# Optimization experiments

Hardware: AMD Instinct MI355X
Metric: run time of the kernel (lower is better)

## Reference

```python
import jax, jax.numpy as jnp
import numpy as np

D, H, DH, FF = 768, 12, 64, 3072

def setup_inputs() -> dict:
    key = jax.random.key(0)
    ks = iter(jax.random.split(key, 40))
    B, Li, Lt = 128, 197, 64
    nrm = lambda shape, s=0.02: (jax.random.normal(next(ks), shape, jnp.float32) * s)
    inp = {}
    inp['image_feats'] = jax.random.normal(next(ks), (B, Li, D), jnp.float32)
    inp['image_att_score'] = jax.random.uniform(next(ks), (B, Li), jnp.float32)
    inp['text_feats'] = jax.random.normal(next(ks), (B, Lt, D), jnp.float32)
    inp['text_att_score'] = jax.random.uniform(next(ks), (B, Lt), jnp.float32)
    inp['tokens'] = jax.random.randint(next(ks), (B, Lt), 0, 1000)
    # BatchNorm1d bottlenecks (inference: running stats)
    for p in ('img', 'txt'):
        inp[f'bn_{p}_g'] = jnp.ones((D,), jnp.float32)
        inp[f'bn_{p}_b'] = jnp.zeros((D,), jnp.float32)
        inp[f'bn_{p}_m'] = nrm((D,), 0.1)
        inp[f'bn_{p}_v'] = jax.random.uniform(next(ks), (D,), jnp.float32, 0.5, 1.5)
    # ResidualAttention (1 layer, cross): ln1, ln2, qkv/out proj, mlp 768->3072->768
    inp['ln1_g'] = jnp.ones((D,), jnp.float32); inp['ln1_b'] = jnp.zeros((D,), jnp.float32)
    inp['ln2_g'] = jnp.ones((D,), jnp.float32); inp['ln2_b'] = jnp.zeros((D,), jnp.float32)
    for n in ('Wq', 'Wk', 'Wv', 'Wo'):
        inp[n] = nrm((D, D))
    for n in ('bq', 'bk', 'bv', 'bo'):
        inp[n] = jnp.zeros((D,), jnp.float32)
    inp['W1'] = nrm((D, FF)); inp['b1'] = jnp.zeros((FF,), jnp.float32)
    inp['W2'] = nrm((FF, D)); inp['b2'] = jnp.zeros((D,), jnp.float32)
    inp['img_K'] = 59   # int(197 * 0.3)
    inp['text_K'] = 19  # int(64 * 0.3)
    return inp

def _ln(x, g, b):
    mu = jnp.mean(x, -1, keepdims=True)
    v = jnp.mean((x - mu) ** 2, -1, keepdims=True)
    return (x - mu) * jax.lax.rsqrt(v + 1e-5) * g + b

def _bn(x, g, b, m, v):
    return (x - m) * jax.lax.rsqrt(v + 1e-5) * g + b

def _cross_block(x, y, key_mask, ln1_g, ln1_b, ln2_g, ln2_b,
                 Wq, bq, Wk, bk, Wv, bv, Wo, bo, W1, b1, W2, b2):
    # cross-attn: queries from x, keys/values from y; pre-LN residual block
    B, Lq, _ = x.shape
    Lk = y.shape[1]
    qn = _ln(x, ln1_g, ln1_b)
    kn = _ln(y, ln1_g, ln1_b)
    q = (qn @ Wq + bq).reshape(B, Lq, H, DH)
    k = (kn @ Wk + bk).reshape(B, Lk, H, DH)
    v = (kn @ Wv + bv).reshape(B, Lk, H, DH)
    scores = jnp.einsum('bqhd,bkhd->bhqk', q, k) / np.float32(np.sqrt(DH))
    if key_mask is not None:  # True = padding -> masked out
        scores = jnp.where(key_mask[:, None, None, :], jnp.float32(-1e9), scores)
    a = jax.nn.softmax(scores, axis=-1)
    att = jnp.einsum('bhqk,bkhd->bqhd', a, v).reshape(B, Lq, D) @ Wo + bo
    x = x + att
    h = _ln(x, ln2_g, ln2_b)
    x = x + jax.nn.gelu(h @ W1 + b1, approximate=False) @ W2 + b2
    return x

def _select(feats, score, K):
    # zero CLS score, full descending sort via top_k, gather token subsets
    L = score.shape[1]
    score = score * jnp.concatenate([jnp.zeros_like(score[:, :1]), jnp.ones_like(score[:, 1:])], axis=1)
    _, idx = jax.lax.top_k(score, L)  # [B, L] sorted desc
    cls = feats[:, :1, :]
    sel1 = jnp.take_along_axis(feats, idx[:, :K, None], axis=1)
    sel2 = jnp.take_along_axis(feats, idx[:, K:2 * K, None], axis=1)
    return jnp.concatenate([cls, sel1], 1), jnp.concatenate([cls, sel2], 1)

def reference(image_feats, image_att_score, text_feats, text_att_score, tokens,
              bn_img_g, bn_img_b, bn_img_m, bn_img_v,
              bn_txt_g, bn_txt_b, bn_txt_m, bn_txt_v,
              ln1_g, ln1_b, ln2_g, ln2_b,
              Wq, bq, Wk, bk, Wv, bv, Wo, bo, W1, b1, W2, b2,
              img_K, text_K):
    blk = lambda x, y, m: _cross_block(x, y, m, ln1_g, ln1_b, ln2_g, ln2_b,
                                       Wq, bq, Wk, bk, Wv, bv, Wo, bo, W1, b1, W2, b2)
    img_global = _bn(image_feats[:, 0, :], bn_img_g, bn_img_b, bn_img_m, bn_img_v)
    text_global = _bn(text_feats[:, 0, :], bn_txt_g, bn_txt_b, bn_txt_m, bn_txt_v)
    text_masks = (tokens == 0)  # True where padding
    img_sel1, img_sel2 = _select(image_feats, image_att_score, img_K)
    image_part1 = blk(img_sel1, image_feats, None)
    image_part2 = blk(img_sel2, image_feats, None)
    txt_sel1, txt_sel2 = _select(text_feats, text_att_score, text_K)
    text_part1 = blk(txt_sel1, text_feats, text_masks)
    text_part2 = blk(txt_sel2, text_feats, text_masks)
    return (img_global, text_global, image_part1, image_part2, text_part1, text_part2)
```

## Files before the change

kernel.cpp:

```cpp
#include <hip/hip_runtime.h>

typedef unsigned short u16;
typedef __bf16 bf16x8 __attribute__((ext_vector_type(8)));
typedef float f32x4 __attribute__((ext_vector_type(4)));

__device__ __forceinline__ float b2f(u16 u) { return __builtin_bit_cast(float, (unsigned)u << 16); }
__device__ __forceinline__ u16 f2b(float f) {
  unsigned x = __builtin_bit_cast(unsigned, f);
  x += 0x7fffu + ((x >> 16) & 1u);
  return (u16)(x >> 16);
}

__device__ __forceinline__ void gload16(const u16* g, u16* l) {
  auto gp = (__attribute__((address_space(1))) void*)(void*)const_cast<u16*>(g);
  auto lp = (__attribute__((address_space(3))) void*)(void*)l;
  __builtin_amdgcn_global_load_lds(gp, lp, 16, 0, 0);
}

__device__ __forceinline__ f32x4 mfma16(bf16x8 a, bf16x8 b, f32x4 c) {
  return __builtin_amdgcn_mfma_f32_16x16x32_bf16(a, b, c, 0, 0, 0);
}

__device__ __forceinline__ float gelu_fast(float v) {
  float u = v * (0.7978845608028654f + 0.03567740813636141f * v * v);
  float e = __expf(2.0f * u);
  float th = 1.0f - 2.0f / (e + 1.0f);
  return 0.5f * v * (1.0f + th);
}

__global__ __launch_bounds__(256) void transpose_k(const float* __restrict__ in, u16* __restrict__ out,
                                                   int R, int C) {
  __shared__ float tile[32][33];
  const int bx = blockIdx.x * 32, by = blockIdx.y * 32;
  const int x = threadIdx.x;
  for (int yy = threadIdx.y; yy < 32; yy += 8) tile[yy][x] = in[(size_t)(by + yy) * C + bx + x];
  __syncthreads();
  for (int yy = threadIdx.y; yy < 32; yy += 8) out[(size_t)(bx + yy) * R + by + x] = f2b(tile[x][yy]);
}

__global__ __launch_bounds__(256) void transpose4(const float* __restrict__ i0, const float* __restrict__ i1,
                                                  const float* __restrict__ i2, const float* __restrict__ i3,
                                                  u16* __restrict__ o0, u16* __restrict__ o1,
                                                  u16* __restrict__ o2, u16* __restrict__ o3) {
  __shared__ float tile[32][33];
  const int z = blockIdx.z;
  const float* in = (z == 0) ? i0 : (z == 1) ? i1 : (z == 2) ? i2 : i3;
  u16* out = (z == 0) ? o0 : (z == 1) ? o1 : (z == 2) ? o2 : o3;
  const int bx = blockIdx.x * 32, by = blockIdx.y * 32;
  const int x = threadIdx.x;
  for (int yy = threadIdx.y; yy < 32; yy += 8) tile[yy][x] = in[(size_t)(by + yy) * 768 + bx + x];
  __syncthreads();
  for (int yy = threadIdx.y; yy < 32; yy += 8) out[(size_t)(bx + yy) * 768 + by + x] = f2b(tile[x][yy]);
}

__global__ __launch_bounds__(256) void bn_kernel(const float* __restrict__ feats, int Lrow,
                                                 const float* g, const float* b, const float* m, const float* v,
                                                 float* __restrict__ out) {
  const int bb = blockIdx.x;
  const float* row = feats + (size_t)bb * Lrow * 768;
  for (int d = threadIdx.x; d < 768; d += 256) {
    float x = row[d];
    out[bb * 768 + d] = (x - m[d]) * (1.0f / sqrtf(v[d] + 1e-5f)) * g[d] + b[d];
  }
}

__global__ __launch_bounds__(256) void topk_sel(const float* __restrict__ score, int L, int Ksel,
                                                int* __restrict__ sel, int Lq) {
  __shared__ float s[256];
  const int b = blockIdx.x;
  const int stride2 = 128 * Lq;
  for (int i = threadIdx.x; i < L; i += 256) {
    float v = score[b * L + i];
    s[i] = (i == 0) ? 0.0f : v;
  }
  __syncthreads();
  for (int i = threadIdx.x; i < L; i += 256) {
    float si = s[i];
    int rank = 0;
    for (int j = 0; j < L; ++j) {
      float sj = s[j];
      rank += (sj > si) || (sj == si && j < i);
    }
    if (rank < Ksel) sel[b * Lq + rank + 1] = i;
    else if (rank < 2 * Ksel) sel[stride2 + b * Lq + (rank - Ksel) + 1] = i;
  }
  if (threadIdx.x == 0) { sel[b * Lq] = 0; sel[stride2 + b * Lq] = 0; }
}

__global__ __launch_bounds__(256) void ln_rows(const float* __restrict__ x, const float* g, const float* b,
                                               u16* __restrict__ out) {
  const int row = blockIdx.x * 4 + (threadIdx.x >> 6);
  const int l = threadIdx.x & 63;
  const float* xr = x + (size_t)row * 768;
  float v[12]; float s = 0.f;
#pragma unroll
  for (int i = 0; i < 12; ++i) { v[i] = xr[l + i * 64]; s += v[i]; }
  for (int d = 1; d < 64; d <<= 1) s += __shfl_xor(s, d);
  const float mu = s * (1.0f / 768.0f);
  float q = 0.f;
#pragma unroll
  for (int i = 0; i < 12; ++i) { float t = v[i] - mu; q += t * t; }
  for (int d = 1; d < 64; d <<= 1) q += __shfl_xor(q, d);
  const float rs = 1.0f / sqrtf(q * (1.0f / 768.0f) + 1e-5f);
#pragma unroll
  for (int i = 0; i < 12; ++i) {
    int c = l + i * 64;
    out[(size_t)row * 768 + c] = f2b((v[i] - mu) * rs * g[c] + b[c]);
  }
}

__global__ __launch_bounds__(128) void gather_kernel(const int* __restrict__ sel, const u16* __restrict__ kn,
                                                     const float* __restrict__ feats, u16* __restrict__ qn,
                                                     float* __restrict__ xs, int Lq, int Lsrc) {
  const int q = blockIdx.x, by = blockIdx.y;
  const int p = by >> 7, b = by & 127;
  const int row = (p * 128 + b) * Lq + q;
  const int src = sel[row];
  const uint4* sq = (const uint4*)(kn + ((size_t)b * Lsrc + src) * 768);
  uint4* dq = (uint4*)(qn + (size_t)row * 768);
  for (int c = threadIdx.x; c < 96; c += 128) dq[c] = sq[c];
  const float4* sx = (const float4*)(feats + ((size_t)b * Lsrc + src) * 768);
  float4* dx = (float4*)(xs + (size_t)row * 768);
  for (int c = threadIdx.x; c < 192; c += 128) dx[c] = sx[c];
}

enum { EPI_PLAIN = 0, EPI_QSCALE = 1, EPI_GELU = 2, EPI_RES_FADD = 3, EPI_RES_OUT = 4 };

template <int EPI>
__device__ __forceinline__ void epi_write(float v, size_t off, void* outp, const float* res) {
  if constexpr (EPI == EPI_QSCALE) {
    ((u16*)outp)[off] = f2b(v * 0.125f);
  } else if constexpr (EPI == EPI_GELU) {
    ((u16*)outp)[off] = f2b(gelu_fast(v));
  } else if constexpr (EPI == EPI_RES_FADD || EPI == EPI_RES_OUT) {
    ((float*)outp)[off] = v + res[off];
  } else {
    ((u16*)outp)[off] = f2b(v);
  }
}

template <int EPI>
__global__ __launch_bounds__(256, 3) void gemm_bt(const u16* __restrict__ A, const u16* __restrict__ Bt,
                                                  const float* __restrict__ bias, const float* __restrict__ res,
                                                  void* __restrict__ outp, int M, int N, int K) {
  __shared__ alignas(16) u16 As[2][4096];
  __shared__ alignas(16) u16 Bs[2][4096];
  const int tid = threadIdx.x, l = tid & 63, w = tid >> 6;
  const int nwg = gridDim.x * gridDim.y;
  int lin = blockIdx.y * gridDim.x + blockIdx.x;
  const int q8 = nwg >> 3, r8 = nwg & 7;
  const int xcd = lin & 7, pos = lin >> 3;
  const int nl = (xcd < r8) ? (xcd * (q8 + 1) + pos) : (r8 * (q8 + 1) + (xcd - r8) * q8 + pos);
  const int m0 = (nl / gridDim.x) * 128, n0 = (nl % gridDim.x) * 128;
  const int wm = (w & 1) * 64, wn = (w >> 1) * 64;
  f32x4 acc[4][4] = {};

  int arow_g[2], ach_g[2];
#pragma unroll
  for (int p = 0; p < 2; ++p) {
    const int s = p * 256 + tid;
    const int rl = s >> 3, v = (s & 7) ^ (rl & 7);
    arow_g[p] = (v >> 2) * 64 + rl;
    ach_g[p] = (v & 3) * 8;
  }
  auto STAGE = [&](int buf, int k0) {
#pragma unroll
    for (int p = 0; p < 2; ++p) {
      const int s = p * 256 + tid;
      gload16(A + (size_t)(m0 + arow_g[p]) * K + k0 + ach_g[p], &As[buf][s * 8]);
      gload16(Bt + (size_t)(n0 + arow_g[p]) * K + k0 + ach_g[p], &Bs[buf][s * 8]);
    }
  };

  const int c = l >> 4;
  auto COMPUTE = [&](int buf) {
    bf16x8 af[4], bfr[4];
#pragma unroll
    for (int i = 0; i < 4; ++i) {
      const int arow = wm + i * 16 + (l & 15);
      const int slot = (c | ((arow >> 6) << 2)) ^ (arow & 7);
      af[i] = *(const bf16x8*)&As[buf][(arow & 63) * 64 + slot * 8];
      const int brow = wn + i * 16 + (l & 15);
      const int slotb = (c | ((brow >> 6) << 2)) ^ (brow & 7);
      bfr[i] = *(const bf16x8*)&Bs[buf][(brow & 63) * 64 + slotb * 8];
    }
    __builtin_amdgcn_s_setprio(1);
#pragma unroll
    for (int mi = 0; mi < 4; ++mi)
#pragma unroll
      for (int ni = 0; ni < 4; ++ni) acc[mi][ni] = mfma16(af[mi], bfr[ni], acc[mi][ni]);
    __builtin_amdgcn_s_setprio(0);
  };

  const int NT = K >> 5;
  STAGE(0, 0);
  int cur = 0;
  for (int t = 0; t < NT - 1; ++t) {
    STAGE(cur ^ 1, (t + 1) << 5);
    asm volatile("s_waitcnt vmcnt(4)" ::: "memory");
    __builtin_amdgcn_sched_barrier(0);
    __builtin_amdgcn_s_barrier();
    COMPUTE(cur);
    __builtin_amdgcn_s_barrier();
    cur ^= 1;
  }
  asm volatile("s_waitcnt vmcnt(0)" ::: "memory");
  __builtin_amdgcn_sched_barrier(0);
  __builtin_amdgcn_s_barrier();
  COMPUTE(cur);

  const int r4 = (l >> 4) * 4, c16 = l & 15;
#pragma unroll
  for (int mi = 0; mi < 4; ++mi)
#pragma unroll
    for (int ni = 0; ni < 4; ++ni) {
      const int gn = n0 + wn + ni * 16 + c16;
      const float bia = bias[gn];
#pragma unroll
      for (int j = 0; j < 4; ++j) {
        const int gm = m0 + wm + mi * 16 + r4 + j;
        epi_write<EPI>(acc[mi][ni][j] + bia, (size_t)gm * N + gn, outp, res);
      }
    }
}

template <int LQP, int LKP, int LQ, int LK, bool MASK>
__global__ __launch_bounds__(256) void attn2(const u16* __restrict__ Q, const u16* __restrict__ KVb,
                                             const int* __restrict__ toks, u16* __restrict__ O) {
  constexpr int LKS = LKP + 8;
  const int h = blockIdx.x, by = blockIdx.y;
  const int p = by & 1, bb = by >> 1;
  const int tid = threadIdx.x, l = tid & 63, w = tid >> 6;
  const size_t qrow0 = (size_t)(p * 128 + bb) * LQ;
  const u16* Qg = Q + qrow0 * 768 + h * 64;
  const u16* Kg = KVb + (size_t)bb * LK * 1536 + h * 64;
  const u16* Vg = Kg + 768;

  __shared__ alignas(16) u16 Qs[LQP * 64];
  __shared__ alignas(16) u16 KV[64 * LKS];
  __shared__ alignas(16) u16 Ss[LQP * LKS];
  __shared__ int tokLds[MASK ? LKP : 1];

  for (int s = tid; s < LQP * 8; s += 256) {
    int row = s >> 3, d8 = (s & 7) ^ (row & 7);
    int gr = row < LQ ? row : LQ - 1;
    gload16(Qg + (size_t)gr * 768 + d8 * 8, &Qs[s * 8]);
  }
  for (int s = tid; s < LKP * 8; s += 256) {
    int row = s >> 3, d8 = (s & 7) ^ (row & 7);
    int gr = row < LK ? row : LK - 1;
    gload16(Kg + (size_t)gr * 1536 + d8 * 8, &KV[s * 8]);
  }
  if (MASK)
    for (int c = tid; c < LKP; c += 256) tokLds[c] = (c < LK) ? toks[bb * LK + c] : 1;
  __syncthreads();

  for (int nt = w; nt < LKP / 16; nt += 4) {
    const int brow = nt * 16 + (l & 15);
#pragma unroll
    for (int mt = 0; mt < LQP / 16; ++mt) {
      const int arow = mt * 16 + (l & 15);
      f32x4 a_ = {0.f, 0.f, 0.f, 0.f};
#pragma unroll
      for (int kk = 0; kk < 2; ++kk) {
        bf16x8 av = *(const bf16x8*)&Qs[arow * 64 + (((kk * 4 + (l >> 4)) ^ (arow & 7)) << 3)];
        bf16x8 bv = *(const bf16x8*)&KV[brow * 64 + (((kk * 4 + (l >> 4)) ^ (brow & 7)) << 3)];
        a_ = mfma16(av, bv, a_);
      }
      const int r0 = mt * 16 + (l >> 4) * 4, cc = nt * 16 + (l & 15);
#pragma unroll
      for (int j = 0; j < 4; ++j) Ss[(r0 + j) * LKS + cc] = f2b(a_[j]);
    }
  }
  __syncthreads();

  {
    const int kcol = tid & 31, d8 = tid >> 5;
#pragma unroll
    for (int kb = 0; kb < LKP / 32; ++kb) {
      const int k = kb * 32 + kcol;
      alignas(16) u16 tmp[8] = {0, 0, 0, 0, 0, 0, 0, 0};
      if (k < LK) *(uint4*)tmp = *(const uint4*)(Vg + (size_t)k * 1536 + d8 * 8);
#pragma unroll
      for (int j = 0; j < 8; ++j) KV[(d8 * 8 + j) * LKS + k] = tmp[j];
    }
  }
  constexpr int NCH = (LKP + 63) / 64;
  for (int r = w; r < LQ; r += 4) {
    float sv[NCH];
    float mx = -INFINITY;
#pragma unroll
    for (int i = 0; i < NCH; ++i) {
      int c = l + (i << 6);
      float s = -INFINITY;
      if (c < LK) {
        s = b2f(Ss[r * LKS + c]);
        if (MASK && tokLds[c] == 0) s = -1e9f;
      }
      sv[i] = s;
      mx = fmaxf(mx, s);
    }
    for (int d = 1; d < 64; d <<= 1) mx = fmaxf(mx, __shfl_xor(mx, d));
    float sum = 0.f;
#pragma unroll
    for (int i = 0; i < NCH; ++i) { float e = __expf(sv[i] - mx); sv[i] = e; sum += e; }
    for (int d = 1; d < 64; d <<= 1) sum += __shfl_xor(sum, d);
    const float inv = 1.0f / sum;
#pragma unroll
    for (int i = 0; i < NCH; ++i) {
      int c = l + (i << 6);
      if (c < LKP) Ss[r * LKS + c] = f2b(sv[i] * inv);
    }
  }
  __syncthreads();

  for (int mt = w; mt < LQP / 16; mt += 4) {
    const int arow = mt * 16 + (l & 15);
#pragma unroll
    for (int nt = 0; nt < 4; ++nt) {
      f32x4 a_ = {0.f, 0.f, 0.f, 0.f};
#pragma unroll
      for (int kk = 0; kk < LKP; kk += 32) {
        bf16x8 av = *(const bf16x8*)&Ss[arow * LKS + kk + (l >> 4) * 8];
        bf16x8 bv = *(const bf16x8*)&KV[(nt * 16 + (l & 15)) * LKS + kk + (l >> 4) * 8];
        a_ = mfma16(av, bv, a_);
      }
      const int r0 = mt * 16 + (l >> 4) * 4, c16 = l & 15;
#pragma unroll
      for (int j = 0; j < 4; ++j) {
        int r = r0 + j;
        if (r < LQ) O[(qrow0 + r) * 768 + h * 64 + nt * 16 + c16] = f2b(a_[j]);
      }
    }
  }
}

extern "C" void kernel_launch(void* const* d_in, const int* in_sizes, int n_in,
                              void* d_out, int out_size, void* d_ws, size_t ws_size,
                              hipStream_t stream) {
  (void)in_sizes; (void)n_in; (void)out_size; (void)ws_size;
  const float* image_feats = (const float*)d_in[0];
  const float* image_att = (const float*)d_in[1];
  const float* text_feats = (const float*)d_in[2];
  const float* text_att = (const float*)d_in[3];
  const int* tokens = (const int*)d_in[4];
  const float* bn_img_g = (const float*)d_in[5];
  const float* bn_img_b = (const float*)d_in[6];
  const float* bn_img_m = (const float*)d_in[7];
  const float* bn_img_v = (const float*)d_in[8];
  const float* bn_txt_g = (const float*)d_in[9];
  const float* bn_txt_b = (const float*)d_in[10];
  const float* bn_txt_m = (const float*)d_in[11];
  const float* bn_txt_v = (const float*)d_in[12];
  const float* ln1_g = (const float*)d_in[13];
  const float* ln1_b = (const float*)d_in[14];
  const float* ln2_g = (const float*)d_in[15];
  const float* ln2_b = (const float*)d_in[16];
  const float* Wq = (const float*)d_in[17];
  const float* Wk = (const float*)d_in[18];
  const float* Wv = (const float*)d_in[19];
  const float* Wo = (const float*)d_in[20];
  const float* bq = (const float*)d_in[21];
  const float* bk = (const float*)d_in[22];
  const float* bv = (const float*)d_in[23];
  const float* bo = (const float*)d_in[24];
  const float* W1 = (const float*)d_in[25];
  const float* b1 = (const float*)d_in[26];
  const float* W2 = (const float*)d_in[27];
  const float* b2 = (const float*)d_in[28];

  float* out = (float*)d_out;
  char* wsp = (char*)d_ws;
  size_t off = 0;
  auto alloc = [&](size_t bytes) -> void* {
    void* p = wsp + off;
    off += (bytes + 255) & ~(size_t)255;
    return p;
  };
  u16* WqT = (u16*)alloc(768 * 768 * 2);
  u16* WkvT = (u16*)alloc((size_t)1536 * 768 * 2);
  u16* WoT = (u16*)alloc(768 * 768 * 2);
  u16* W1T = (u16*)alloc((size_t)768 * 3072 * 2);
  u16* W2T = (u16*)alloc((size_t)768 * 3072 * 2);
  float* bkv = (float*)alloc(1536 * 4);
  char* kvbase = (char*)(wsp + off);
  u16* kn_i = (u16*)alloc((size_t)25216 * 768 * 2);
  u16* KVb_i = (u16*)alloc((size_t)25216 * 1536 * 2);
  u16* kn_t = (u16*)alloc((size_t)8192 * 768 * 2);
  u16* KVb_t = (u16*)alloc((size_t)8192 * 1536 * 2);
  u16* gb = (u16*)kvbase;
  int* sel_i = (int*)alloc(2 * 128 * 60 * 4);
  int* sel_t = (int*)alloc(2 * 128 * 20 * 4);
  u16* qn = (u16*)alloc((size_t)20480 * 768 * 2);
  float* xs = (float*)alloc((size_t)20480 * 768 * 4);
  u16* Qb = (u16*)alloc((size_t)20480 * 768 * 2);

  const dim3 tb(32, 8);
  transpose4<<<dim3(24, 24, 4), tb, 0, stream>>>(Wq, Wk, Wv, Wo, WqT, WkvT, WkvT + (size_t)768 * 768, WoT);
  transpose_k<<<dim3(96, 24), tb, 0, stream>>>(W1, W1T, 768, 3072);
  transpose_k<<<dim3(24, 96), tb, 0, stream>>>(W2, W2T, 3072, 768);
  hipMemcpyAsync(bkv, bk, 768 * 4, hipMemcpyDeviceToDevice, stream);
  hipMemcpyAsync(bkv + 768, bv, 768 * 4, hipMemcpyDeviceToDevice, stream);

  bn_kernel<<<128, 256, 0, stream>>>(image_feats, 197, bn_img_g, bn_img_b, bn_img_m, bn_img_v, out);
  bn_kernel<<<128, 256, 0, stream>>>(text_feats, 64, bn_txt_g, bn_txt_b, bn_txt_m, bn_txt_v, out + 98304);

  topk_sel<<<128, 256, 0, stream>>>(image_att, 197, 59, sel_i, 60);
  topk_sel<<<128, 256, 0, stream>>>(text_att, 64, 19, sel_t, 20);

  ln_rows<<<25216 / 4, 256, 0, stream>>>(image_feats, ln1_g, ln1_b, kn_i);
  gemm_bt<EPI_PLAIN><<<dim3(12, 197), 256, 0, stream>>>(kn_i, WkvT, bkv, nullptr, KVb_i, 25216, 1536, 768);
  ln_rows<<<8192 / 4, 256, 0, stream>>>(text_feats, ln1_g, ln1_b, kn_t);
  gemm_bt<EPI_PLAIN><<<dim3(12, 64), 256, 0, stream>>>(kn_t, WkvT, bkv, nullptr, KVb_t, 8192, 1536, 768);

  gather_kernel<<<dim3(60, 256), 128, 0, stream>>>(sel_i, kn_i, image_feats, qn, xs, 60, 197);
  gather_kernel<<<dim3(20, 256), 128, 0, stream>>>(sel_t, kn_t, text_feats, qn + (size_t)15360 * 768,
                                                   xs + (size_t)15360 * 768, 20, 64);

  gemm_bt<EPI_QSCALE><<<dim3(6, 160), 256, 0, stream>>>(qn, WqT, bq, nullptr, Qb, 20480, 768, 768);

  attn2<64, 224, 60, 197, false><<<dim3(12, 256), 256, 0, stream>>>(Qb, KVb_i, nullptr, qn);
  attn2<32, 64, 20, 64, true><<<dim3(12, 256), 256, 0, stream>>>(Qb + (size_t)15360 * 768, KVb_t,
                                                                 tokens, qn + (size_t)15360 * 768);

  gemm_bt<EPI_RES_FADD><<<dim3(6, 160), 256, 0, stream>>>(qn, WoT, bo, xs, xs, 20480, 768, 768);
  ln_rows<<<20480 / 4, 256, 0, stream>>>(xs, ln2_g, ln2_b, Qb);
  gemm_bt<EPI_GELU><<<dim3(24, 160), 256, 0, stream>>>(Qb, W1T, b1, nullptr, gb, 20480, 3072, 768);
  gemm_bt<EPI_RES_OUT><<<dim3(6, 160), 256, 0, stream>>>(gb, W2T, b2, xs, out + 196608, 20480, 768, 3072);
}
```

Before: 742.5 us.

## Triple-buffer GEMM LDS pipeline and merge image/text KV projections into one launch

The GEMM main loop moves from double to triple buffering in LDS, issuing loads two k-steps ahead with adjusted vmcnt waits, so more memory latency is hidden behind MFMA work. The image and text KV projection GEMMs now share one contiguous buffer and run as a single launch of 33408 rows, which removes a launch and the tail of the smaller grid. In exchange, LDS per block grows from 32KB to 48KB, which may limit how many blocks fit per CU under the launch bound of 3.

```diff
diff --git a/kernel.cpp b/kernel.cpp
--- a/kernel.cpp
+++ b/kernel.cpp
@@ -143,8 +143,8 @@
 __global__ __launch_bounds__(256, 3) void gemm_bt(const u16* __restrict__ A, const u16* __restrict__ Bt,
                                                   const float* __restrict__ bias, const float* __restrict__ res,
                                                   void* __restrict__ outp, int M, int N, int K) {
-  __shared__ alignas(16) u16 As[2][4096];
-  __shared__ alignas(16) u16 Bs[2][4096];
+  __shared__ alignas(16) u16 As[3][4096];
+  __shared__ alignas(16) u16 Bs[3][4096];
   const int tid = threadIdx.x, l = tid & 63, w = tid >> 6;
   const int nwg = gridDim.x * gridDim.y;
   int lin = blockIdx.y * gridDim.x + blockIdx.x;
@@ -194,20 +194,23 @@
 
   const int NT = K >> 5;
   STAGE(0, 0);
-  int cur = 0;
-  for (int t = 0; t < NT - 1; ++t) {
-    STAGE(cur ^ 1, (t + 1) << 5);
-    asm volatile("s_waitcnt vmcnt(4)" ::: "memory");
+  if (NT > 1) STAGE(1, 32);
+  int b0 = 0;
+  for (int t = 0; t < NT; ++t) {
+    if (t + 2 < NT) {
+      STAGE((b0 == 0) ? 2 : b0 - 1, (t + 2) << 5);
+      asm volatile("s_waitcnt vmcnt(8)" ::: "memory");
+    } else if (t + 1 < NT) {
+      asm volatile("s_waitcnt vmcnt(4)" ::: "memory");
+    } else {
+      asm volatile("s_waitcnt vmcnt(0)" ::: "memory");
+    }
     __builtin_amdgcn_sched_barrier(0);
     __builtin_amdgcn_s_barrier();
-    COMPUTE(cur);
+    COMPUTE(b0);
     __builtin_amdgcn_s_barrier();
-    cur ^= 1;
-  }
-  asm volatile("s_waitcnt vmcnt(0)" ::: "memory");
-  __builtin_amdgcn_sched_barrier(0);
-  __builtin_amdgcn_s_barrier();
-  COMPUTE(cur);
+    b0 = (b0 == 2) ? 0 : b0 + 1;
+  }
 
   const int r4 = (l >> 4) * 4, c16 = l & 15;
 #pragma unroll
@@ -384,10 +387,10 @@
   u16* W2T = (u16*)alloc((size_t)768 * 3072 * 2);
   float* bkv = (float*)alloc(1536 * 4);
   char* kvbase = (char*)(wsp + off);
-  u16* kn_i = (u16*)alloc((size_t)25216 * 768 * 2);
-  u16* KVb_i = (u16*)alloc((size_t)25216 * 1536 * 2);
-  u16* kn_t = (u16*)alloc((size_t)8192 * 768 * 2);
-  u16* KVb_t = (u16*)alloc((size_t)8192 * 1536 * 2);
+  u16* kn = (u16*)alloc((size_t)33408 * 768 * 2);
+  u16* KVb = (u16*)alloc((size_t)33408 * 1536 * 2);
+  u16* kn_t = kn + (size_t)25216 * 768;
+  u16* KVb_t = KVb + (size_t)25216 * 1536;
   u16* gb = (u16*)kvbase;
   int* sel_i = (int*)alloc(2 * 128 * 60 * 4);
   int* sel_t = (int*)alloc(2 * 128 * 20 * 4);
@@ -408,18 +411,17 @@
   topk_sel<<<128, 256, 0, stream>>>(image_att, 197, 59, sel_i, 60);
   topk_sel<<<128, 256, 0, stream>>>(text_att, 64, 19, sel_t, 20);
 
-  ln_rows<<<25216 / 4, 256, 0, stream>>>(image_feats, ln1_g, ln1_b, kn_i);
-  gemm_bt<EPI_PLAIN><<<dim3(12, 197), 256, 0, stream>>>(kn_i, WkvT, bkv, nullptr, KVb_i, 25216, 1536, 768);
+  ln_rows<<<25216 / 4, 256, 0, stream>>>(image_feats, ln1_g, ln1_b, kn);
   ln_rows<<<8192 / 4, 256, 0, stream>>>(text_feats, ln1_g, ln1_b, kn_t);
-  gemm_bt<EPI_PLAIN><<<dim3(12, 64), 256, 0, stream>>>(kn_t, WkvT, bkv, nullptr, KVb_t, 8192, 1536, 768);
-
-  gather_kernel<<<dim3(60, 256), 128, 0, stream>>>(sel_i, kn_i, image_feats, qn, xs, 60, 197);
+  gemm_bt<EPI_PLAIN><<<dim3(12, 261), 256, 0, stream>>>(kn, WkvT, bkv, nullptr, KVb, 33408, 1536, 768);
+
+  gather_kernel<<<dim3(60, 256), 128, 0, stream>>>(sel_i, kn, image_feats, qn, xs, 60, 197);
   gather_kernel<<<dim3(20, 256), 128, 0, stream>>>(sel_t, kn_t, text_feats, qn + (size_t)15360 * 768,
                                                    xs + (size_t)15360 * 768, 20, 64);
 
   gemm_bt<EPI_QSCALE><<<dim3(6, 160), 256, 0, stream>>>(qn, WqT, bq, nullptr, Qb, 20480, 768, 768);
 
-  attn2<64, 224, 60, 197, false><<<dim3(12, 256), 256, 0, stream>>>(Qb, KVb_i, nullptr, qn);
+  attn2<64, 224, 60, 197, false><<<dim3(12, 256), 256, 0, stream>>>(Qb, KVb, nullptr, qn);
   attn2<32, 64, 20, 64, true><<<dim3(12, 256), 256, 0, stream>>>(Qb + (size_t)15360 * 768, KVb_t,
                                                                  tokens, qn + (size_t)15360 * 768);
 
```

After: 777.6 us. 4.7% more time.
